# Kernel optimization log

Measured on AMD Instinct MI355X. Metric: run time of the kernel, lower is better.

## Reference

```python
import jax, jax.numpy as jnp
import numpy as np

B, T, N, D = 16, 12, 10000, 2
E = 320000


def setup_inputs() -> dict:
    key = jax.random.key(0)
    k1, k2, k3 = jax.random.split(key, 3)
    predictions = jax.random.normal(k1, (B, T, N, D), dtype=jnp.float32)
    targets = jax.random.normal(k2, (B, T, N, D), dtype=jnp.float32)
    edge_index = jax.random.randint(k3, (2, E), 0, N, dtype=jnp.int64)
    return {"predictions": predictions, "targets": targets, "edge_index": edge_index}


def reference(predictions, targets, edge_index):
    # weights from __init__ defaults
    mse_w, spatial_w, temporal_w, conservation_w = 1.0, 0.1, 0.05, 0.02

    # main loss: MAE (use_mae=True)
    main_loss = jnp.mean(jnp.abs(predictions - targets))

    # spatial consistency: the per-(b,t) python loop of mse over edges,
    # averaged over batch*pred_len, equals one global mean over [B,T,E,D]
    src, dst = edge_index[0], edge_index[1]
    pred_diff = jnp.abs(predictions[:, :, src] - predictions[:, :, dst])  # [B,T,E,D]
    targ_diff = jnp.abs(targets[:, :, src] - targets[:, :, dst])
    spatial_loss = jnp.mean((pred_diff - targ_diff) ** 2)

    # temporal smoothness: first-order time differences
    pd_t = predictions[:, 1:] - predictions[:, :-1]
    td_t = targets[:, 1:] - targets[:, :-1]
    temporal_loss = jnp.mean((pd_t - td_t) ** 2)

    # conservation: sum over nodes
    pred_sum = predictions.sum(axis=2)  # [B,T,D]
    targ_sum = targets.sum(axis=2)
    conservation_loss = jnp.mean((pred_sum - targ_sum) ** 2)

    total_loss = (mse_w * main_loss + spatial_w * spatial_loss
                  + temporal_w * temporal_loss + conservation_w * conservation_loss)

    # order: loss, main_loss, spatial_loss, temporal_loss, conservation_loss
    return jnp.stack([total_loss, main_loss, spatial_loss, temporal_loss, conservation_loss])
```

## Files before the change

### kernel.cpp

```cpp
#include <hip/hip_runtime.h>

#define BB 16
#define TT 12
#define NN 10000
#define DD 2
#define EE 320000
#define BT 192
#define TOT 3840000
#define SLICE 20000

#define NCH 96
#define SLICES 16
#define EPS 20000
#define SPATB (NCH*SLICES)

#define PACKB 942
#define STRB 1536
#define EOFFB 1250
#define PREPG (PACKB + STRB + EOFFB)

#define EOFF_BOFF 32768
#define W2_BOFF   1314816
#define NEED (W2_BOFF + (size_t)NCH * NN * 2 * 4)

typedef float v2f __attribute__((ext_vector_type(2)));
typedef _Float16 h2 __attribute__((ext_vector_type(2)));

__device__ __forceinline__ h2 habs2v(h2 x) {
    unsigned u = __builtin_bit_cast(unsigned, x) & 0x7FFF7FFFu;
    return __builtin_bit_cast(h2, u);
}
__device__ __forceinline__ h2 pkh(float a, float b) {
#if defined(__has_builtin)
#if __has_builtin(__builtin_amdgcn_cvt_pkrtz)
    return __builtin_bit_cast(h2, __builtin_amdgcn_cvt_pkrtz(a, b));
#else
    h2 r; r[0] = (_Float16)a; r[1] = (_Float16)b; return r;
#endif
#else
    h2 r; r[0] = (_Float16)a; r[1] = (_Float16)b; return r;
#endif
}
__device__ __forceinline__ void slot_acc(unsigned a, unsigned b, h2& acc) {
    v2f ap = __builtin_amdgcn_cvt_pk_f32_fp8((int)a, false);
    v2f at = __builtin_amdgcn_cvt_pk_f32_fp8((int)a, true);
    v2f bp = __builtin_amdgcn_cvt_pk_f32_fp8((int)b, false);
    v2f bq = __builtin_amdgcn_cvt_pk_f32_fp8((int)b, true);
    h2 d = habs2v(pkh(ap[0], ap[1]) - pkh(bp[0], bp[1]))
         - habs2v(pkh(at[0], at[1]) - pkh(bq[0], bq[1]));
    acc = d * d + acc;
}

__device__ __forceinline__ void stream_body(int b, const float* __restrict__ p,
                                            const float* __restrict__ tg,
                                            float* __restrict__ ws) {
    int bt = b >> 3, part = b & 7;
    int tt = bt % TT;
    size_t base = (size_t)bt * SLICE;
    bool inner = (tt < TT - 1);
    float m = 0.f, w = 0.f, c = 0.f;
    int j0 = part * 2500;
    for (int j = j0 + threadIdx.x; j < j0 + 2500; j += 256) {
        size_t jj = base + j;
        float pv = p[jj], tv = tg[jj];
        m += fabsf(pv - tv);
        c += pv - tv;
        if (inner) {
            float pn = p[jj + SLICE], tn = tg[jj + SLICE];
            float dd = (pn - pv) - (tn - tv);
            w += dd * dd;
        }
    }
    for (int o = 32; o >= 2; o >>= 1) {
        m += __shfl_xor(m, o); w += __shfl_xor(w, o); c += __shfl_xor(c, o);
    }
    m += __shfl_xor(m, 1);
    w += __shfl_xor(w, 1);
    __shared__ float sm[4], sw[4], s0[4], s1[4];
    int wid = threadIdx.x >> 6, lane = threadIdx.x & 63;
    if (lane == 0) { sm[wid] = m; sw[wid] = w; s0[wid] = c; }
    if (lane == 1) { s1[wid] = c; }
    __syncthreads();
    if (threadIdx.x == 0) {
        float a = 0, bv = 0, c0 = 0, c1 = 0;
        for (int k = 0; k < 4; k++) { a += sm[k]; bv += sw[k]; c0 += s0[k]; c1 += s1[k]; }
        ws[b] = a; ws[1536 + b] = bv;
        ws[3072 + 2 * b] = c0; ws[3072 + 2 * b + 1] = c1;
    }
}

__global__ __launch_bounds__(256) void prep_kernel(const float* __restrict__ p,
                                                   const float* __restrict__ tg,
                                                   const int* __restrict__ idx,
                                                   char* __restrict__ wsb) {
    float* ws = (float*)wsb;
    int g = blockIdx.x;
    if (g < PACKB) {
        __shared__ unsigned tile[64][33];
        int ng = g / 6, cg = g % 6;
        int n0 = ng * 64;
        int ln = threadIdx.x & 63, r = threadIdx.x >> 6;
        int n = n0 + ln;
        if (n < NN) {
            for (int sl = r; sl < 32; sl += 4) {
                int bt = cg * 32 + sl;
                size_t e = (size_t)bt * SLICE + (size_t)n * 2;
                float2 pv = *reinterpret_cast<const float2*>(p + e);
                float2 tv = *reinterpret_cast<const float2*>(tg + e);
                int pk = __builtin_amdgcn_cvt_pk_fp8_f32(pv.x, pv.y, 0, false);
                pk = __builtin_amdgcn_cvt_pk_fp8_f32(tv.x, tv.y, pk, true);
                tile[ln][sl] = (unsigned)pk;
            }
        }
        __syncthreads();
        unsigned* w2c = (unsigned*)(wsb + W2_BOFF);
        for (int f = threadIdx.x; f < 2048; f += 256) {
            int c2 = f >> 7;
            int j2 = f & 127;
            int nn2 = j2 >> 1, k2 = j2 & 1;
            int n2 = n0 + nn2;
            if (n2 < NN) {
                int c = cg * 16 + c2;
                w2c[((unsigned)(c * NN + n2) << 1) + k2] = tile[nn2][c2 * 2 + k2];
            }
        }
    } else if (g < PACKB + STRB) {
        stream_body(g - PACKB, p, tg, ws);
    } else {
        int e = (g - PACKB - STRB) * 256 + threadIdx.x;
        if (e < EE) {
            unsigned* eoff = (unsigned*)(wsb + EOFF_BOFF);
            eoff[e] = (unsigned)idx[e] | ((unsigned)idx[EE + e] << 16);
        }
    }
}

__global__ __launch_bounds__(1024, 8) void spatial_kernel(const uint2* __restrict__ w2c2,
                                                          const unsigned* __restrict__ eoff,
                                                          float* __restrict__ ws) {
    __shared__ uint2 nd[NN];
    __shared__ float red[16];
    int bid = blockIdx.x;
    int c = bid % NCH;
    int s = bid / NCH;
    const uint4* src4 = (const uint4*)(w2c2 + (size_t)c * NN);
    uint4* nd4 = (uint4*)nd;
    for (int i = threadIdx.x; i < NN / 2; i += 1024)
        nd4[i] = src4[i];
    __syncthreads();

    int e = s * EPS + threadIdx.x;
    const int eend = s * EPS + EPS;
    h2 acc0 = (h2)0, acc1 = (h2)0;
    while (e + 1024 < eend) {
        unsigned eo1 = eoff[e], eo2 = eoff[e + 1024];
        uint2 A1 = nd[eo1 & 0xFFFFu], B1 = nd[eo1 >> 16];
        uint2 A2 = nd[eo2 & 0xFFFFu], B2 = nd[eo2 >> 16];
        slot_acc(A1.x, B1.x, acc0);
        slot_acc(A1.y, B1.y, acc1);
        slot_acc(A2.x, B2.x, acc0);
        slot_acc(A2.y, B2.y, acc1);
        e += 2048;
    }
    if (e < eend) {
        unsigned eo = eoff[e];
        uint2 A = nd[eo & 0xFFFFu], B = nd[eo >> 16];
        slot_acc(A.x, B.x, acc0);
        slot_acc(A.y, B.y, acc1);
    }
    float acc = (float)acc0[0] + (float)acc0[1] + (float)acc1[0] + (float)acc1[1];
    for (int o = 32; o; o >>= 1) acc += __shfl_xor(acc, o);
    if ((threadIdx.x & 63) == 0) red[threadIdx.x >> 6] = acc;
    __syncthreads();
    if (threadIdx.x == 0) {
        float t = 0.f;
        for (int k = 0; k < 16; ++k) t += red[k];
        ws[6144 + bid] = t;
    }
}

__global__ __launch_bounds__(256) void spatial_fb(const float* __restrict__ p,
                                                  const float* __restrict__ tg,
                                                  const int* __restrict__ idx,
                                                  float* __restrict__ ws) {
    int lane = threadIdx.x & 63;
    int wave = (blockIdx.x * 256 + threadIdx.x) >> 6;
    float s = 0.f;
    for (int e = wave; e < EE; e += SPATB * 4) {
        int sn = idx[e] * DD, dn = idx[EE + e] * DD;
        for (int bt = lane; bt < BT; bt += 64) {
            size_t base = (size_t)bt * SLICE;
            float2 ps = *reinterpret_cast<const float2*>(p + base + sn);
            float2 pd = *reinterpret_cast<const float2*>(p + base + dn);
            float2 ts = *reinterpret_cast<const float2*>(tg + base + sn);
            float2 td = *reinterpret_cast<const float2*>(tg + base + dn);
            float d0 = fabsf(ps.x - pd.x) - fabsf(ts.x - td.x);
            float d1 = fabsf(ps.y - pd.y) - fabsf(ts.y - td.y);
            s = fmaf(d0, d0, s);
            s = fmaf(d1, d1, s);
        }
    }
    for (int o = 32; o; o >>= 1) s += __shfl_xor(s, o);
    __shared__ float sv[4];
    if (lane == 0) sv[threadIdx.x >> 6] = s;
    __syncthreads();
    if (threadIdx.x == 0) ws[6144 + blockIdx.x] = sv[0] + sv[1] + sv[2] + sv[3];
}

__global__ __launch_bounds__(256) void stream_fb(const float* __restrict__ p,
                                                 const float* __restrict__ tg,
                                                 float* __restrict__ ws) {
    stream_body(blockIdx.x, p, tg, ws);
}

__global__ __launch_bounds__(1024) void finalize_kernel(const float* __restrict__ ws,
                                                        float* __restrict__ out) {
    int tid = threadIdx.x;
    float a = 0, bv = 0, sp = 0, cq = 0;
    for (int k = tid; k < STRB; k += 1024) { a += ws[k]; bv += ws[1536 + k]; }
    for (int k = tid; k < SPATB; k += 1024) sp += ws[6144 + k];
    if (tid < BT * DD) {
        int bt = tid >> 1, par = tid & 1;
        float cs = 0;
        for (int part = 0; part < 8; ++part)
            cs += ws[3072 + ((bt * 8 + part) << 1) + par];
        cq = cs * cs;
    }
    for (int o = 32; o; o >>= 1) {
        a += __shfl_xor(a, o); bv += __shfl_xor(bv, o);
        sp += __shfl_xor(sp, o); cq += __shfl_xor(cq, o);
    }
    __shared__ float ra[16], rb[16], rs[16], rc[16];
    int wid = tid >> 6;
    if ((tid & 63) == 0) { ra[wid] = a; rb[wid] = bv; rs[wid] = sp; rc[wid] = cq; }
    __syncthreads();
    if (tid == 0) {
        float A = 0, B2 = 0, S = 0, C = 0;
        for (int k = 0; k < 16; k++) { A += ra[k]; B2 += rb[k]; S += rs[k]; C += rc[k]; }
        float mainl = A / (float)TOT;
        float temp  = B2 / (float)(BB * (TT - 1) * NN * DD);
        float spat  = S / ((float)BT * (float)EE * (float)DD);
        float cons  = C / (float)(BT * DD);
        out[0] = mainl + 0.1f * spat + 0.05f * temp + 0.02f * cons;
        out[1] = mainl; out[2] = spat; out[3] = temp; out[4] = cons;
    }
}

extern "C" void kernel_launch(void* const* d_in, const int* in_sizes, int n_in,
                              void* d_out, int out_size, void* d_ws, size_t ws_size,
                              hipStream_t stream) {
    const float* p  = (const float*)d_in[0];
    const float* tg = (const float*)d_in[1];
    const int*   ix = (const int*)d_in[2];
    float* out = (float*)d_out;
    char*  wsb = (char*)d_ws;
    float* ws  = (float*)d_ws;

    if (ws_size >= NEED) {
        prep_kernel<<<PREPG, 256, 0, stream>>>(p, tg, ix, wsb);
        spatial_kernel<<<SPATB, 1024, 0, stream>>>((const uint2*)(wsb + W2_BOFF),
                                                   (const unsigned*)(wsb + EOFF_BOFF), ws);
    } else {
        stream_fb<<<STRB, 256, 0, stream>>>(p, tg, ws);
        spatial_fb<<<SPATB, 256, 0, stream>>>(p, tg, ix, ws);
    }
    finalize_kernel<<<1, 1024, 0, stream>>>(ws, out);
}
```

Baseline: 57.42 us.

## Move dense stream reductions from prep kernel into spatial kernel extra blocks

The MAE, temporal and conservation reductions leave the prep kernel and run as 192 extra 1024-thread blocks appended to the spatial kernel's grid, one per (b,t) slice, using float2 loads. The idea is to shorten the prep kernel, which sits on the critical path before the spatial gather, and overlap the dense streaming with the LDS-bound spatial work. Finalize now reads one partial per slice instead of eight. The half-precision arithmetic is rewritten with __half2 intrinsics. The trade-off is that the 192 stream blocks reserve 1024-thread slots sized for the spatial kernel's large shared array, and they may be scheduled last, leaving a tail at the end of the spatial kernel.

```diff
diff --git a/kernel.cpp b/kernel.cpp
--- a/kernel.cpp
+++ b/kernel.cpp
@@ -1,4 +1,5 @@
 #include <hip/hip_runtime.h>
+#include <hip/hip_fp16.h>
 
 #define BB 16
 #define TT 12
@@ -13,87 +14,36 @@
 #define SLICES 16
 #define EPS 20000
 #define SPATB (NCH*SLICES)
+#define SPATG (SPATB + BT)
 
 #define PACKB 942
-#define STRB 1536
 #define EOFFB 1250
-#define PREPG (PACKB + STRB + EOFFB)
+#define PREPG (PACKB + EOFFB)
 
 #define EOFF_BOFF 32768
 #define W2_BOFF   1314816
 #define NEED (W2_BOFF + (size_t)NCH * NN * 2 * 4)
 
 typedef float v2f __attribute__((ext_vector_type(2)));
-typedef _Float16 h2 __attribute__((ext_vector_type(2)));
-
-__device__ __forceinline__ h2 habs2v(h2 x) {
-    unsigned u = __builtin_bit_cast(unsigned, x) & 0x7FFF7FFFu;
-    return __builtin_bit_cast(h2, u);
-}
-__device__ __forceinline__ h2 pkh(float a, float b) {
-#if defined(__has_builtin)
-#if __has_builtin(__builtin_amdgcn_cvt_pkrtz)
-    return __builtin_bit_cast(h2, __builtin_amdgcn_cvt_pkrtz(a, b));
-#else
-    h2 r; r[0] = (_Float16)a; r[1] = (_Float16)b; return r;
-#endif
-#else
-    h2 r; r[0] = (_Float16)a; r[1] = (_Float16)b; return r;
-#endif
-}
-__device__ __forceinline__ void slot_acc(unsigned a, unsigned b, h2& acc) {
+
+__device__ __forceinline__ __half2 pkh2(float a, float b) {
+    auto t = __builtin_amdgcn_cvt_pkrtz(a, b);
+    return *reinterpret_cast<__half2*>(&t);
+}
+__device__ __forceinline__ void slot_acc(unsigned a, unsigned b, __half2& acc) {
     v2f ap = __builtin_amdgcn_cvt_pk_f32_fp8((int)a, false);
     v2f at = __builtin_amdgcn_cvt_pk_f32_fp8((int)a, true);
     v2f bp = __builtin_amdgcn_cvt_pk_f32_fp8((int)b, false);
     v2f bq = __builtin_amdgcn_cvt_pk_f32_fp8((int)b, true);
-    h2 d = habs2v(pkh(ap[0], ap[1]) - pkh(bp[0], bp[1]))
-         - habs2v(pkh(at[0], at[1]) - pkh(bq[0], bq[1]));
-    acc = d * d + acc;
-}
-
-__device__ __forceinline__ void stream_body(int b, const float* __restrict__ p,
-                                            const float* __restrict__ tg,
-                                            float* __restrict__ ws) {
-    int bt = b >> 3, part = b & 7;
-    int tt = bt % TT;
-    size_t base = (size_t)bt * SLICE;
-    bool inner = (tt < TT - 1);
-    float m = 0.f, w = 0.f, c = 0.f;
-    int j0 = part * 2500;
-    for (int j = j0 + threadIdx.x; j < j0 + 2500; j += 256) {
-        size_t jj = base + j;
-        float pv = p[jj], tv = tg[jj];
-        m += fabsf(pv - tv);
-        c += pv - tv;
-        if (inner) {
-            float pn = p[jj + SLICE], tn = tg[jj + SLICE];
-            float dd = (pn - pv) - (tn - tv);
-            w += dd * dd;
-        }
-    }
-    for (int o = 32; o >= 2; o >>= 1) {
-        m += __shfl_xor(m, o); w += __shfl_xor(w, o); c += __shfl_xor(c, o);
-    }
-    m += __shfl_xor(m, 1);
-    w += __shfl_xor(w, 1);
-    __shared__ float sm[4], sw[4], s0[4], s1[4];
-    int wid = threadIdx.x >> 6, lane = threadIdx.x & 63;
-    if (lane == 0) { sm[wid] = m; sw[wid] = w; s0[wid] = c; }
-    if (lane == 1) { s1[wid] = c; }
-    __syncthreads();
-    if (threadIdx.x == 0) {
-        float a = 0, bv = 0, c0 = 0, c1 = 0;
-        for (int k = 0; k < 4; k++) { a += sm[k]; bv += sw[k]; c0 += s0[k]; c1 += s1[k]; }
-        ws[b] = a; ws[1536 + b] = bv;
-        ws[3072 + 2 * b] = c0; ws[3072 + 2 * b + 1] = c1;
-    }
+    __half2 d = __hsub2(__habs2(__hsub2(pkh2(ap[0], ap[1]), pkh2(bp[0], bp[1]))),
+                        __habs2(__hsub2(pkh2(at[0], at[1]), pkh2(bq[0], bq[1]))));
+    acc = __hfma2(d, d, acc);
 }
 
 __global__ __launch_bounds__(256) void prep_kernel(const float* __restrict__ p,
                                                    const float* __restrict__ tg,
                                                    const int* __restrict__ idx,
                                                    char* __restrict__ wsb) {
-    float* ws = (float*)wsb;
     int g = blockIdx.x;
     if (g < PACKB) {
         __shared__ unsigned tile[64][33];
@@ -115,8 +65,7 @@
         __syncthreads();
         unsigned* w2c = (unsigned*)(wsb + W2_BOFF);
         for (int f = threadIdx.x; f < 2048; f += 256) {
-            int c2 = f >> 7;
-            int j2 = f & 127;
+            int c2 = f >> 7, j2 = f & 127;
             int nn2 = j2 >> 1, k2 = j2 & 1;
             int n2 = n0 + nn2;
             if (n2 < NN) {
@@ -124,10 +73,8 @@
                 w2c[((unsigned)(c * NN + n2) << 1) + k2] = tile[nn2][c2 * 2 + k2];
             }
         }
-    } else if (g < PACKB + STRB) {
-        stream_body(g - PACKB, p, tg, ws);
     } else {
-        int e = (g - PACKB - STRB) * 256 + threadIdx.x;
+        int e = (g - PACKB) * 256 + threadIdx.x;
         if (e < EE) {
             unsigned* eoff = (unsigned*)(wsb + EOFF_BOFF);
             eoff[e] = (unsigned)idx[e] | ((unsigned)idx[EE + e] << 16);
@@ -137,21 +84,69 @@
 
 __global__ __launch_bounds__(1024, 8) void spatial_kernel(const uint2* __restrict__ w2c2,
                                                           const unsigned* __restrict__ eoff,
+                                                          const float* __restrict__ p,
+                                                          const float* __restrict__ tg,
                                                           float* __restrict__ ws) {
     __shared__ uint2 nd[NN];
-    __shared__ float red[16];
+    __shared__ float red[64];
     int bid = blockIdx.x;
+    int tid = threadIdx.x;
+
+    if (bid >= SPATB) {
+        int bt = bid - SPATB;
+        size_t base = (size_t)bt * SLICE;
+        bool inner = (bt % TT) < TT - 1;
+        const float2* p2  = (const float2*)(p + base);
+        const float2* t2  = (const float2*)(tg + base);
+        const float2* pn2 = (const float2*)(p + base + SLICE);
+        const float2* tn2 = (const float2*)(tg + base + SLICE);
+        float m = 0.f, w = 0.f, cx = 0.f, cy = 0.f;
+        for (int j = tid; j < NN; j += 1024) {
+            float2 pv = p2[j], tv = t2[j];
+            m += fabsf(pv.x - tv.x) + fabsf(pv.y - tv.y);
+            cx += pv.x - tv.x;
+            cy += pv.y - tv.y;
+            if (inner) {
+                float2 pn = pn2[j], tn = tn2[j];
+                float d0 = (pn.x - pv.x) - (tn.x - tv.x);
+                float d1 = (pn.y - pv.y) - (tn.y - tv.y);
+                w = fmaf(d0, d0, w);
+                w = fmaf(d1, d1, w);
+            }
+        }
+        for (int o = 32; o; o >>= 1) {
+            m += __shfl_xor(m, o); w += __shfl_xor(w, o);
+            cx += __shfl_xor(cx, o); cy += __shfl_xor(cy, o);
+        }
+        int wid = tid >> 6;
+        if ((tid & 63) == 0) {
+            red[wid] = m; red[16 + wid] = w; red[32 + wid] = cx; red[48 + wid] = cy;
+        }
+        __syncthreads();
+        if (tid == 0) {
+            float M = 0, W = 0, CX = 0, CY = 0;
+            for (int k = 0; k < 16; ++k) {
+                M += red[k]; W += red[16 + k]; CX += red[32 + k]; CY += red[48 + k];
+            }
+            ws[bt] = M;
+            ws[1536 + bt] = W;
+            ws[3072 + 2 * bt] = CX;
+            ws[3072 + 2 * bt + 1] = CY;
+        }
+        return;
+    }
+
     int c = bid % NCH;
     int s = bid / NCH;
     const uint4* src4 = (const uint4*)(w2c2 + (size_t)c * NN);
     uint4* nd4 = (uint4*)nd;
-    for (int i = threadIdx.x; i < NN / 2; i += 1024)
+    for (int i = tid; i < NN / 2; i += 1024)
         nd4[i] = src4[i];
     __syncthreads();
 
-    int e = s * EPS + threadIdx.x;
+    int e = s * EPS + tid;
     const int eend = s * EPS + EPS;
-    h2 acc0 = (h2)0, acc1 = (h2)0;
+    __half2 acc0 = __float2half2_rn(0.f), acc1 = __float2half2_rn(0.f);
     while (e + 1024 < eend) {
         unsigned eo1 = eoff[e], eo2 = eoff[e + 1024];
         uint2 A1 = nd[eo1 & 0xFFFFu], B1 = nd[eo1 >> 16];
@@ -168,14 +163,81 @@
         slot_acc(A.x, B.x, acc0);
         slot_acc(A.y, B.y, acc1);
     }
-    float acc = (float)acc0[0] + (float)acc0[1] + (float)acc1[0] + (float)acc1[1];
+    float acc = __low2float(acc0) + __high2float(acc0)
+              + __low2float(acc1) + __high2float(acc1);
     for (int o = 32; o; o >>= 1) acc += __shfl_xor(acc, o);
-    if ((threadIdx.x & 63) == 0) red[threadIdx.x >> 6] = acc;
-    __syncthreads();
-    if (threadIdx.x == 0) {
+    if ((tid & 63) == 0) red[tid >> 6] = acc;
+    __syncthreads();
+    if (tid == 0) {
         float t = 0.f;
         for (int k = 0; k < 16; ++k) t += red[k];
         ws[6144 + bid] = t;
+    }
+}
+
+__global__ __launch_bounds__(1024) void finalize_kernel(const float* __restrict__ ws,
+                                                        float* __restrict__ out) {
+    int tid = threadIdx.x;
+    float a = 0, bv = 0, sp = 0, cq = 0;
+    if (tid < BT) { a = ws[tid]; bv = ws[1536 + tid]; }
+    for (int k = tid; k < SPATB; k += 1024) sp += ws[6144 + k];
+    if (tid < BT * DD) { float cs = ws[3072 + tid]; cq = cs * cs; }
+    for (int o = 32; o; o >>= 1) {
+        a += __shfl_xor(a, o); bv += __shfl_xor(bv, o);
+        sp += __shfl_xor(sp, o); cq += __shfl_xor(cq, o);
+    }
+    __shared__ float ra[16], rb[16], rs[16], rc[16];
+    int wid = tid >> 6;
+    if ((tid & 63) == 0) { ra[wid] = a; rb[wid] = bv; rs[wid] = sp; rc[wid] = cq; }
+    __syncthreads();
+    if (tid == 0) {
+        float A = 0, B2 = 0, S = 0, C = 0;
+        for (int k = 0; k < 16; k++) { A += ra[k]; B2 += rb[k]; S += rs[k]; C += rc[k]; }
+        float mainl = A / (float)TOT;
+        float temp  = B2 / (float)(BB * (TT - 1) * NN * DD);
+        float spat  = S / ((float)BT * (float)EE * (float)DD);
+        float cons  = C / (float)(BT * DD);
+        out[0] = mainl + 0.1f * spat + 0.05f * temp + 0.02f * cons;
+        out[1] = mainl; out[2] = spat; out[3] = temp; out[4] = cons;
+    }
+}
+
+__global__ __launch_bounds__(256) void stream_fb(const float* __restrict__ p,
+                                                 const float* __restrict__ tg,
+                                                 float* __restrict__ ws) {
+    int b = blockIdx.x;
+    int bt = b >> 3, part = b & 7;
+    int tt = bt % TT;
+    size_t base = (size_t)bt * SLICE;
+    bool inner = (tt < TT - 1);
+    float m = 0.f, w = 0.f, c = 0.f;
+    int j0 = part * 2500;
+    for (int j = j0 + threadIdx.x; j < j0 + 2500; j += 256) {
+        size_t jj = base + j;
+        float pv = p[jj], tv = tg[jj];
+        m += fabsf(pv - tv);
+        c += pv - tv;
+        if (inner) {
+            float pn = p[jj + SLICE], tn = tg[jj + SLICE];
+            float dd = (pn - pv) - (tn - tv);
+            w += dd * dd;
+        }
+    }
+    for (int o = 32; o >= 2; o >>= 1) {
+        m += __shfl_xor(m, o); w += __shfl_xor(w, o); c += __shfl_xor(c, o);
+    }
+    m += __shfl_xor(m, 1);
+    w += __shfl_xor(w, 1);
+    __shared__ float sm[4], sw[4], s0[4], s1[4];
+    int wid = threadIdx.x >> 6, lane = threadIdx.x & 63;
+    if (lane == 0) { sm[wid] = m; sw[wid] = w; s0[wid] = c; }
+    if (lane == 1) { s1[wid] = c; }
+    __syncthreads();
+    if (threadIdx.x == 0) {
+        float a = 0, bv = 0, c0 = 0, c1 = 0;
+        for (int k = 0; k < 4; k++) { a += sm[k]; bv += sw[k]; c0 += s0[k]; c1 += s1[k]; }
+        ws[b] = a; ws[1536 + b] = bv;
+        ws[3072 + 2 * b] = c0; ws[3072 + 2 * b + 1] = c1;
     }
 }
 
@@ -207,17 +269,11 @@
     if (threadIdx.x == 0) ws[6144 + blockIdx.x] = sv[0] + sv[1] + sv[2] + sv[3];
 }
 
-__global__ __launch_bounds__(256) void stream_fb(const float* __restrict__ p,
-                                                 const float* __restrict__ tg,
-                                                 float* __restrict__ ws) {
-    stream_body(blockIdx.x, p, tg, ws);
-}
-
-__global__ __launch_bounds__(1024) void finalize_kernel(const float* __restrict__ ws,
-                                                        float* __restrict__ out) {
+__global__ __launch_bounds__(1024) void finalize_fb(const float* __restrict__ ws,
+                                                    float* __restrict__ out) {
     int tid = threadIdx.x;
     float a = 0, bv = 0, sp = 0, cq = 0;
-    for (int k = tid; k < STRB; k += 1024) { a += ws[k]; bv += ws[1536 + k]; }
+    for (int k = tid; k < 1536; k += 1024) { a += ws[k]; bv += ws[1536 + k]; }
     for (int k = tid; k < SPATB; k += 1024) sp += ws[6144 + k];
     if (tid < BT * DD) {
         int bt = tid >> 1, par = tid & 1;
@@ -258,11 +314,13 @@
 
     if (ws_size >= NEED) {
         prep_kernel<<<PREPG, 256, 0, stream>>>(p, tg, ix, wsb);
-        spatial_kernel<<<SPATB, 1024, 0, stream>>>((const uint2*)(wsb + W2_BOFF),
-                                                   (const unsigned*)(wsb + EOFF_BOFF), ws);
+        spatial_kernel<<<SPATG, 1024, 0, stream>>>((const uint2*)(wsb + W2_BOFF),
+                                                   (const unsigned*)(wsb + EOFF_BOFF),
+                                                   p, tg, ws);
+        finalize_kernel<<<1, 1024, 0, stream>>>(ws, out);
     } else {
-        stream_fb<<<STRB, 256, 0, stream>>>(p, tg, ws);
+        stream_fb<<<1536, 256, 0, stream>>>(p, tg, ws);
         spatial_fb<<<SPATB, 256, 0, stream>>>(p, tg, ix, ws);
-    }
-    finalize_kernel<<<1, 1024, 0, stream>>>(ws, out);
-}
+        finalize_fb<<<1, 1024, 0, stream>>>(ws, out);
+    }
+}
```

After: 55.75 us. 1.03x faster.
